# Performance work log

Hardware: AMD Instinct MI355X
Metric: run time of the kernel (lower is better)

## Reference

```python
import jax, jax.numpy as jnp
import numpy as np

DIM = 2048
BATCH = 16384
EPS = 1e-12


def setup_inputs() -> dict:
    key = jax.random.key(0)
    ks = jax.random.split(key, 12)
    d = DIM
    inp = {
        "h_final": jax.random.normal(ks[0], (BATCH, d), dtype=jnp.float32),
        "v_claim": jax.random.normal(ks[1], (BATCH, d), dtype=jnp.float32),
        "v_doc": jax.random.normal(ks[2], (BATCH, d), dtype=jnp.float32),
        # feature_extractor: Linear(d+3, d) -> ReLU -> Linear(d, d//2) -> ReLU
        "W1": jax.random.normal(ks[3], (d + 3, d), dtype=jnp.float32) / np.sqrt(d + 3),
        "b1": jnp.zeros((d,), dtype=jnp.float32),
        "W2": jax.random.normal(ks[4], (d, d // 2), dtype=jnp.float32) / np.sqrt(d),
        "b2": jnp.zeros((d // 2,), dtype=jnp.float32),
        # retrieval head: Linear(d//2, 1) -> Sigmoid
        "Wr": jax.random.normal(ks[5], (d // 2, 1), dtype=jnp.float32) / np.sqrt(d // 2),
        "br": jnp.zeros((1,), dtype=jnp.float32),
    }
    return inp


def reference(h_final, v_claim, v_doc, W1, b1, W2, b2, Wr, br):
    # L2-normalize claim/doc vectors (F.normalize with eps clamp)
    cn = v_claim / jnp.maximum(jnp.linalg.norm(v_claim, axis=-1, keepdims=True), EPS)
    dn = v_doc / jnp.maximum(jnp.linalg.norm(v_doc, axis=-1, keepdims=True), EPS)
    # alignment = cosine similarity (vectors already unit norm) -> [B, 1]
    align = jnp.sum(cn * dn, axis=-1, keepdims=True)
    # divergence = 1 - alignment; tension = divergence^2
    div = 1.0 - align
    tens = div * div
    features = jnp.concatenate([h_final, align, div, tens], axis=-1)  # [B, d+3]
    h = jax.nn.relu(features @ W1 + b1)
    shared = jax.nn.relu(h @ W2 + b2)  # [B, d//2]
    out = jax.nn.sigmoid(shared @ Wr + br)  # [B, 1] (task='retrieval')
    return out
```

## Files before the change

kernel.cpp:

```cpp
#include <hip/hip_runtime.h>
#include <hip/hip_bf16.h>
#include <stdint.h>

#define BATCH 16384
#define DIM   2048
#define DIM2  1024

typedef __attribute__((ext_vector_type(8))) short short8;
typedef __attribute__((ext_vector_type(4))) float f32x4;

__device__ __forceinline__ ushort f2bf(float f) {
  uint32_t u = __float_as_uint(f);
  u += 0x7fffu + ((u >> 16) & 1u);
  return (ushort)(u >> 16);
}
__device__ __forceinline__ float bf2f(ushort h) {
  return __uint_as_float(((uint32_t)h) << 16);
}

__device__ __forceinline__ void gload_lds16(const void* g, void* l) {
  __builtin_amdgcn_global_load_lds(
      (__attribute__((address_space(1))) void*)g,
      (__attribute__((address_space(3))) void*)l,
      16, 0, 0);
}

__device__ __forceinline__ f32x4 MFMA(short8 a, short8 b, f32x4 c) {
  return __builtin_amdgcn_mfma_f32_16x16x32_bf16(a, b, c, 0, 0, 0);
}

__global__ void __launch_bounds__(256) prep_fused(const float* __restrict__ vc,
                                                  const float* __restrict__ vd,
                                                  const float* __restrict__ h,
                                                  ushort* __restrict__ hbf,
                                                  float* __restrict__ feats) {
  int row = blockIdx.x;
  int t = threadIdx.x;
  const float4* c = (const float4*)(vc + (size_t)row * DIM);
  const float4* d = (const float4*)(vd + (size_t)row * DIM);
  float dot = 0.f, c2 = 0.f, d2 = 0.f;
#pragma unroll
  for (int p = 0; p < 2; ++p) {
    float4 a = c[t * 2 + p];
    float4 b = d[t * 2 + p];
    dot += a.x * b.x + a.y * b.y + a.z * b.z + a.w * b.w;
    c2  += a.x * a.x + a.y * a.y + a.z * a.z + a.w * a.w;
    d2  += b.x * b.x + b.y * b.y + b.z * b.z + b.w * b.w;
  }
  {
    const float4* hp = (const float4*)(h + (size_t)row * DIM);
    float4 f0 = hp[t * 2], f1 = hp[t * 2 + 1];
    uint4 u;
    u.x = (uint32_t)f2bf(f0.x) | ((uint32_t)f2bf(f0.y) << 16);
    u.y = (uint32_t)f2bf(f0.z) | ((uint32_t)f2bf(f0.w) << 16);
    u.z = (uint32_t)f2bf(f1.x) | ((uint32_t)f2bf(f1.y) << 16);
    u.w = (uint32_t)f2bf(f1.z) | ((uint32_t)f2bf(f1.w) << 16);
    ((uint4*)hbf)[(size_t)row * 256 + t] = u;
  }
#pragma unroll
  for (int off = 32; off >= 1; off >>= 1) {
    dot += __shfl_down(dot, off, 64);
    c2  += __shfl_down(c2, off, 64);
    d2  += __shfl_down(d2, off, 64);
  }
  __shared__ float red[3][4];
  int l = t & 63, w = t >> 6;
  if (l == 0) { red[0][w] = dot; red[1][w] = c2; red[2][w] = d2; }
  __syncthreads();
  if (t == 0) {
    float D  = red[0][0] + red[0][1] + red[0][2] + red[0][3];
    float C2 = red[1][0] + red[1][1] + red[1][2] + red[1][3];
    float D2 = red[2][0] + red[2][1] + red[2][2] + red[2][3];
    float nc = fmaxf(sqrtf(C2), 1e-12f);
    float nd = fmaxf(sqrtf(D2), 1e-12f);
    float align = D / (nc * nd);
    float dv = 1.f - align;
    feats[row] = align;
    feats[BATCH + row] = dv;
    feats[2 * BATCH + row] = dv * dv;
  }
}

__global__ void __launch_bounds__(256) transW(const float* __restrict__ W,
                                              ushort* __restrict__ WT,
                                              int K, int N) {
  __shared__ float tile[32][33];
  int t = threadIdx.x;
  int tx = t & 31, ty = t >> 5;
  int c0 = blockIdx.x * 32, r0 = blockIdx.y * 32;
#pragma unroll
  for (int p = 0; p < 4; ++p)
    tile[ty + p * 8][tx] = W[(size_t)(r0 + ty + p * 8) * N + c0 + tx];
  __syncthreads();
#pragma unroll
  for (int p = 0; p < 4; ++p) {
    int rr = ty + p * 8;
    WT[(size_t)(c0 + rr) * K + r0 + tx] = f2bf(tile[tx][rr]);
  }
}

template <int MODE, int N>
__global__ void __launch_bounds__(512, 1) gemm256(const ushort* __restrict__ A,
                                                  const ushort* __restrict__ BT,
                                                  ushort* __restrict__ C,
                                                  const float* __restrict__ feats,
                                                  const float* __restrict__ wex,
                                                  const float* __restrict__ bias) {
  constexpr int K = 2048;
  constexpr int NT = K / 64;
  __shared__ __align__(16) char lds[131072];
  const int tid = threadIdx.x;
  const int l = tid & 63, w = tid >> 6;
  const int wr = w >> 2, wc = w & 3;
  const int l4 = l & 15, lhi = l >> 4;

  constexpr int GX = N / 256;
  const int bid = blockIdx.x;
  const int tx = bid % GX, ty = bid / GX;
  const size_t rowBase = (size_t)ty * 256;
  const int colBase = tx * 256;

  const int swz = (l4 & 7) << 4;
  const int aoffBase = l4 * 128 + ((wr * 64 + lhi * 16) ^ swz);
  const int boffBase = ((wc & 1) * 64 + l4) * 128 + (((wc >> 1) * 64 + lhi * 16) ^ swz);

  const char* pAs[2];
  const char* pBs[2];
#pragma unroll
  for (int c = 0; c < 2; ++c) {
    int o = c * 8192 + tid * 16;
    int r = o >> 7, b0 = o & 127;
    int bsw = b0 ^ ((r & 7) << 4);
    int hb = bsw >> 6, cb = bsw & 63;
    pAs[c] = (const char*)A + (rowBase + hb * 128 + r) * (2 * K) + cb;
    pBs[c] = (const char*)BT + ((size_t)colBase + hb * 128 + r) * (2 * K) + cb;
  }
  const int ldso0 = w * 1024;
  const int ldso1 = 8192 + w * 1024;

#define STAGE(srcT, destPar, M, kh)                                          \
  do {                                                                       \
    char* dst_ = lds + (destPar) * 65536 + (kh) * 32768 + (M) * 16384;       \
    const char* s0_ = ((M) ? pBs[0] : pAs[0]) + (srcT) * 128 + (kh) * 64;    \
    const char* s1_ = ((M) ? pBs[1] : pAs[1]) + (srcT) * 128 + (kh) * 64;    \
    gload_lds16(s0_, dst_ + ldso0);                                          \
    gload_lds16(s1_, dst_ + ldso1);                                          \
    asm volatile("" ::: "memory");                                           \
  } while (0)

#define LOADA(q, d, kh)                                                      \
  do {                                                                       \
    const char* sb_ = lds + (d) * 65536 + (kh) * 32768;                      \
    aq[0] = *(const short8*)(sb_ + ((q) * 4 + 0) * 2048 + aoffBase);         \
    aq[1] = *(const short8*)(sb_ + ((q) * 4 + 1) * 2048 + aoffBase);         \
    aq[2] = *(const short8*)(sb_ + ((q) * 4 + 2) * 2048 + aoffBase);         \
    aq[3] = *(const short8*)(sb_ + ((q) * 4 + 3) * 2048 + aoffBase);         \
  } while (0)

#define LOADB(d, kh)                                                         \
  do {                                                                       \
    const char* sb_ = lds + (d) * 65536 + (kh) * 32768 + 16384;              \
    bq[0] = *(const short8*)(sb_ + 0 * 2048 + boffBase);                     \
    bq[1] = *(const short8*)(sb_ + 1 * 2048 + boffBase);                     \
    bq[2] = *(const short8*)(sb_ + 2 * 2048 + boffBase);                     \
    bq[3] = *(const short8*)(sb_ + 3 * 2048 + boffBase);                     \
  } while (0)

#define MF(q)                                                                \
  do {                                                                       \
    _Pragma("unroll") for (int j_ = 0; j_ < 4; ++j_)                         \
        _Pragma("unroll") for (int n_ = 0; n_ < 4; ++n_)                     \
            acc[(q) * 4 + j_][n_] = MFMA(aq[j_], bq[n_], acc[(q) * 4 + j_][n_]); \
  } while (0)

#define BAR()     __builtin_amdgcn_s_barrier()
#define MEMF()    asm volatile("" ::: "memory")
#define VM8()     asm volatile("s_waitcnt vmcnt(8)" ::: "memory")
#define PRIO(x)   __builtin_amdgcn_s_setprio(x)

  f32x4 acc[8][4];
#pragma unroll
  for (int i = 0; i < 8; ++i)
#pragma unroll
    for (int j = 0; j < 4; ++j) acc[i][j] = (f32x4){0.f, 0.f, 0.f, 0.f};

  STAGE(0, 0, 0, 0);
  STAGE(0, 0, 1, 0);
  STAGE(0, 0, 0, 1);
  STAGE(0, 0, 1, 1);
  STAGE(1, 1, 0, 0);
  STAGE(1, 1, 1, 0);
  VM8();
  BAR();
  MEMF();

  for (int I = 0; I < NT / 2; ++I) {
    const int o = 2 * I + 1;
    const int e2 = (2 * I + 2 < NT) ? 2 * I + 2 : 0;
    const int o2 = (2 * I + 3 < NT) ? 2 * I + 3 : 0;
    short8 aq[4], bq[4];
    LOADB(0, 0);
    LOADA(0, 0, 0);
    STAGE(o, 1, 0, 1);
    BAR(); MEMF();
    PRIO(1); MF(0); PRIO(0);
    BAR(); MEMF();
    LOADA(1, 0, 0);
    STAGE(o, 1, 1, 1);
    BAR(); MEMF();
    PRIO(1); MF(1); PRIO(0);
    VM8();
    BAR(); MEMF();
    LOADB(0, 1);
    LOADA(0, 0, 1);
    STAGE(e2, 0, 0, 0);
    BAR(); MEMF();
    PRIO(1); MF(0); PRIO(0);
    BAR(); MEMF();
    LOADA(1, 0, 1);
    STAGE(e2, 0, 1, 0);
    BAR(); MEMF();
    PRIO(1); MF(1); PRIO(0);
    VM8();
    BAR(); MEMF();
    LOADB(1, 0);
    LOADA(0, 1, 0);
    STAGE(e2, 0, 0, 1);
    BAR(); MEMF();
    PRIO(1); MF(0); PRIO(0);
    BAR(); MEMF();
    LOADA(1, 1, 0);
    STAGE(e2, 0, 1, 1);
    BAR(); MEMF();
    PRIO(1); MF(1); PRIO(0);
    VM8();
    BAR(); MEMF();
    LOADB(1, 1);
    LOADA(0, 1, 1);
    STAGE(o2, 1, 0, 0);
    BAR(); MEMF();
    PRIO(1); MF(0); PRIO(0);
    BAR(); MEMF();
    LOADA(1, 1, 1);
    STAGE(o2, 1, 1, 0);
    BAR(); MEMF();
    PRIO(1); MF(1); PRIO(0);
    VM8();
    BAR(); MEMF();
  }
  asm volatile("s_waitcnt vmcnt(0)" ::: "memory");

  int ccv[4];
  float bb[4], wa[4], wb2[4], wc3[4];
#pragma unroll
  for (int n = 0; n < 4; ++n) {
    int cc = colBase + wc * 64 + n * 16 + l4;
    ccv[n] = cc;
    bb[n] = bias[cc];
    if (MODE == 1) {
      wa[n] = wex[cc]; wb2[n] = wex[2048 + cc]; wc3[n] = wex[4096 + cc];
    } else {
      wa[n] = 0.f; wb2[n] = 0.f; wc3[n] = 0.f;
    }
  }
  const int lhi4 = lhi * 4;
#pragma unroll
  for (int m = 0; m < 8; ++m) {
#pragma unroll
    for (int r = 0; r < 4; ++r) {
      size_t rr = rowBase + wr * 128 + m * 16 + lhi4 + r;
      float f1 = 0.f, f2 = 0.f, f3 = 0.f;
      if (MODE == 1) {
        f1 = feats[rr]; f2 = feats[BATCH + rr]; f3 = feats[2 * BATCH + rr];
      }
#pragma unroll
      for (int n = 0; n < 4; ++n) {
        float v = acc[m][n][r] + bb[n];
        if (MODE == 1) v += f1 * wa[n] + f2 * wb2[n] + f3 * wc3[n];
        v = fmaxf(v, 0.f);
        C[rr * N + ccv[n]] = f2bf(v);
      }
    }
  }
#undef STAGE
#undef LOADA
#undef LOADB
#undef MF
#undef BAR
#undef MEMF
#undef VM8
#undef PRIO
}

__global__ void __launch_bounds__(256) head_kernel(const ushort* __restrict__ S,
                                                   const float* __restrict__ Wr,
                                                   const float* __restrict__ br,
                                                   float* __restrict__ out) {
  int row = blockIdx.x * 4 + (threadIdx.x >> 6);
  int l = threadIdx.x & 63;
  const ushort* s = S + (size_t)row * DIM2 + l * 16;
  const float4* wp = (const float4*)(Wr + l * 16);
  uint4 u0 = *(const uint4*)s;
  uint4 u1 = *(const uint4*)(s + 8);
  float4 w0 = wp[0], w1 = wp[1], w2 = wp[2], w3 = wp[3];
  float sum = 0.f;
  sum += bf2f((ushort)(u0.x & 0xffff)) * w0.x + bf2f((ushort)(u0.x >> 16)) * w0.y;
  sum += bf2f((ushort)(u0.y & 0xffff)) * w0.z + bf2f((ushort)(u0.y >> 16)) * w0.w;
  sum += bf2f((ushort)(u0.z & 0xffff)) * w1.x + bf2f((ushort)(u0.z >> 16)) * w1.y;
  sum += bf2f((ushort)(u0.w & 0xffff)) * w1.z + bf2f((ushort)(u0.w >> 16)) * w1.w;
  sum += bf2f((ushort)(u1.x & 0xffff)) * w2.x + bf2f((ushort)(u1.x >> 16)) * w2.y;
  sum += bf2f((ushort)(u1.y & 0xffff)) * w2.z + bf2f((ushort)(u1.y >> 16)) * w2.w;
  sum += bf2f((ushort)(u1.z & 0xffff)) * w3.x + bf2f((ushort)(u1.z >> 16)) * w3.y;
  sum += bf2f((ushort)(u1.w & 0xffff)) * w3.z + bf2f((ushort)(u1.w >> 16)) * w3.w;
#pragma unroll
  for (int off = 32; off >= 1; off >>= 1) sum += __shfl_down(sum, off, 64);
  if (l == 0) out[row] = 1.f / (1.f + expf(-(sum + br[0])));
}

extern "C" void kernel_launch(void* const* d_in, const int* in_sizes, int n_in,
                              void* d_out, int out_size, void* d_ws, size_t ws_size,
                              hipStream_t stream) {
  const float* h_final = (const float*)d_in[0];
  const float* v_claim = (const float*)d_in[1];
  const float* v_doc   = (const float*)d_in[2];
  const float* W1      = (const float*)d_in[3];
  const float* b1      = (const float*)d_in[4];
  const float* W2      = (const float*)d_in[5];
  const float* b2      = (const float*)d_in[6];
  const float* Wr      = (const float*)d_in[7];
  const float* br      = (const float*)d_in[8];
  float* out = (float*)d_out;

  char* ws = (char*)d_ws;
  ushort* Abf   = (ushort*)ws;
  ushort* Hbf   = (ushort*)(ws + 67108864);
  ushort* W1T   = (ushort*)(ws + 134217728);
  ushort* W2T   = (ushort*)(ws + 142606336);
  float*  feats = (float*)(ws + 146800640);
  ushort* Sbf   = Abf;

  prep_fused<<<BATCH, 256, 0, stream>>>(v_claim, v_doc, h_final, Abf, feats);
  transW<<<dim3(DIM / 32, DIM / 32), 256, 0, stream>>>(W1, W1T, DIM, DIM);
  transW<<<dim3(DIM2 / 32, DIM / 32), 256, 0, stream>>>(W2, W2T, DIM, DIM2);

  gemm256<1, DIM><<<(DIM / 256) * (BATCH / 256), 512, 0, stream>>>(
      Abf, W1T, Hbf, feats, W1 + (size_t)2048 * 2048, b1);
  gemm256<2, DIM2><<<(DIM2 / 256) * (BATCH / 256), 512, 0, stream>>>(
      Hbf, W2T, Sbf, nullptr, nullptr, b2);

  head_kernel<<<BATCH / 4, 256, 0, stream>>>(Sbf, Wr, br, out);
}
```

Before: 294.2 us.

## Process one row per wavefront in prep and remap GEMM tiles per XCD

The prep kernel now assigns one row per 64-lane wavefront, four rows per block. It preloads the h row in registers alongside the claim/doc loads, and reduces with xor shuffles only, so the LDS reduction and block barrier are gone. The GEMM block index is remapped so each of the 8 XCDs handles a contiguous band of 8 row-tiles, which should raise L2 reuse of A rows within an XCD. The mapping assumes 64 row-tiles (BATCH/256) and round-robin dispatch of blocks across XCDs.

```diff
diff --git a/kernel.cpp b/kernel.cpp
--- a/kernel.cpp
+++ b/kernel.cpp
@@ -34,46 +34,40 @@
                                                   const float* __restrict__ h,
                                                   ushort* __restrict__ hbf,
                                                   float* __restrict__ feats) {
-  int row = blockIdx.x;
-  int t = threadIdx.x;
-  const float4* c = (const float4*)(vc + (size_t)row * DIM);
-  const float4* d = (const float4*)(vd + (size_t)row * DIM);
+  const int w = threadIdx.x >> 6, l = threadIdx.x & 63;
+  const int row = blockIdx.x * 4 + w;
+  const float4* c  = (const float4*)(vc + (size_t)row * DIM);
+  const float4* d  = (const float4*)(vd + (size_t)row * DIM);
+  const float4* hp = (const float4*)(h  + (size_t)row * DIM);
   float dot = 0.f, c2 = 0.f, d2 = 0.f;
-#pragma unroll
-  for (int p = 0; p < 2; ++p) {
-    float4 a = c[t * 2 + p];
-    float4 b = d[t * 2 + p];
+  float4 hv[8];
+#pragma unroll
+  for (int j = 0; j < 8; ++j) {
+    float4 a = c[j * 64 + l];
+    float4 b = d[j * 64 + l];
+    hv[j] = hp[j * 64 + l];
     dot += a.x * b.x + a.y * b.y + a.z * b.z + a.w * b.w;
     c2  += a.x * a.x + a.y * a.y + a.z * a.z + a.w * a.w;
     d2  += b.x * b.x + b.y * b.y + b.z * b.z + b.w * b.w;
   }
-  {
-    const float4* hp = (const float4*)(h + (size_t)row * DIM);
-    float4 f0 = hp[t * 2], f1 = hp[t * 2 + 1];
-    uint4 u;
-    u.x = (uint32_t)f2bf(f0.x) | ((uint32_t)f2bf(f0.y) << 16);
-    u.y = (uint32_t)f2bf(f0.z) | ((uint32_t)f2bf(f0.w) << 16);
-    u.z = (uint32_t)f2bf(f1.x) | ((uint32_t)f2bf(f1.y) << 16);
-    u.w = (uint32_t)f2bf(f1.z) | ((uint32_t)f2bf(f1.w) << 16);
-    ((uint4*)hbf)[(size_t)row * 256 + t] = u;
+  uint2* ho = (uint2*)(hbf + (size_t)row * DIM);
+#pragma unroll
+  for (int j = 0; j < 8; ++j) {
+    uint2 u;
+    u.x = (uint32_t)f2bf(hv[j].x) | ((uint32_t)f2bf(hv[j].y) << 16);
+    u.y = (uint32_t)f2bf(hv[j].z) | ((uint32_t)f2bf(hv[j].w) << 16);
+    ho[j * 64 + l] = u;
   }
 #pragma unroll
   for (int off = 32; off >= 1; off >>= 1) {
-    dot += __shfl_down(dot, off, 64);
-    c2  += __shfl_down(c2, off, 64);
-    d2  += __shfl_down(d2, off, 64);
-  }
-  __shared__ float red[3][4];
-  int l = t & 63, w = t >> 6;
-  if (l == 0) { red[0][w] = dot; red[1][w] = c2; red[2][w] = d2; }
-  __syncthreads();
-  if (t == 0) {
-    float D  = red[0][0] + red[0][1] + red[0][2] + red[0][3];
-    float C2 = red[1][0] + red[1][1] + red[1][2] + red[1][3];
-    float D2 = red[2][0] + red[2][1] + red[2][2] + red[2][3];
-    float nc = fmaxf(sqrtf(C2), 1e-12f);
-    float nd = fmaxf(sqrtf(D2), 1e-12f);
-    float align = D / (nc * nd);
+    dot += __shfl_xor(dot, off, 64);
+    c2  += __shfl_xor(c2, off, 64);
+    d2  += __shfl_xor(d2, off, 64);
+  }
+  if (l == 0) {
+    float nc = fmaxf(sqrtf(c2), 1e-12f);
+    float nd = fmaxf(sqrtf(d2), 1e-12f);
+    float align = dot / (nc * nd);
     float dv = 1.f - align;
     feats[row] = align;
     feats[BATCH + row] = dv;
@@ -116,7 +110,10 @@
 
   constexpr int GX = N / 256;
   const int bid = blockIdx.x;
-  const int tx = bid % GX, ty = bid / GX;
+  const int xcd = bid & 7;
+  const int s = bid >> 3;
+  const int tx = s % GX;
+  const int ty = xcd * 8 + s / GX;
   const size_t rowBase = (size_t)ty * 256;
   const int colBase = tx * 256;
 
@@ -339,7 +336,7 @@
   float*  feats = (float*)(ws + 146800640);
   ushort* Sbf   = Abf;
 
-  prep_fused<<<BATCH, 256, 0, stream>>>(v_claim, v_doc, h_final, Abf, feats);
+  prep_fused<<<BATCH / 4, 256, 0, stream>>>(v_claim, v_doc, h_final, Abf, feats);
   transW<<<dim3(DIM / 32, DIM / 32), 256, 0, stream>>>(W1, W1T, DIM, DIM);
   transW<<<dim3(DIM2 / 32, DIM / 32), 256, 0, stream>>>(W2, W2T, DIM, DIM2);
 
```

After: 288.0 us. 2.1% less time.
